# Kernel optimization log

Hardware: AMD Instinct MI355X
Metric: run time of the kernel (lower is better)

Reference implementation:

```python
import jax, jax.numpy as jnp
import numpy as np

N_NODES = 100000
N_EDGES = 1600000
N_FEAT = 128
N_HID = 128
N_CLASS = 10
N_GRAPHS = 512
BN_EPS = 1e-5


def setup_inputs() -> dict:
    key = jax.random.key(0)
    ks = jax.random.split(key, 12)
    x = jax.random.normal(ks[0], (N_NODES, N_FEAT), dtype=jnp.float32)
    edge_index = jax.random.randint(ks[1], (2, N_EDGES), 0, N_NODES, dtype=jnp.int32)
    batch = jnp.sort(jax.random.randint(ks[2], (N_NODES,), 0, N_GRAPHS, dtype=jnp.int32))
    s1 = 1.0 / np.sqrt(N_FEAT)
    s2 = 1.0 / np.sqrt(N_HID)
    W1 = jax.random.uniform(ks[3], (N_FEAT, N_HID), jnp.float32, -s1, s1)
    b1 = jax.random.uniform(ks[4], (N_HID,), jnp.float32, -s1, s1)
    gamma = jnp.ones((N_HID,), jnp.float32)
    beta = jnp.zeros((N_HID,), jnp.float32)
    W2 = jax.random.uniform(ks[5], (N_HID, N_HID), jnp.float32, -s2, s2)
    b2 = jax.random.uniform(ks[6], (N_HID,), jnp.float32, -s2, s2)
    clsW = jax.random.uniform(ks[7], (N_HID, N_CLASS), jnp.float32, -s2, s2)
    clsb = jax.random.uniform(ks[8], (N_CLASS,), jnp.float32, -s2, s2)
    return {"x": x, "edge_index": edge_index, "batch": batch,
            "W1": W1, "b1": b1, "gamma": gamma, "beta": beta,
            "W2": W2, "b2": b2, "clsW": clsW, "clsb": clsb}


def _gcn_norm(edge_index, n_nodes):
    # add self-loops, compute symmetric normalization D^-1/2 A_hat D^-1/2
    loops = jnp.arange(n_nodes, dtype=edge_index.dtype)
    src = jnp.concatenate([edge_index[0], loops])
    dst = jnp.concatenate([edge_index[1], loops])
    deg = jax.ops.segment_sum(jnp.ones_like(dst, dtype=jnp.float32), dst,
                              num_segments=n_nodes)
    dinv = jnp.where(deg > 0, jax.lax.rsqrt(deg), 0.0)
    norm = dinv[src] * dinv[dst]  # [E + N]
    return src, dst, norm


def _gcn_conv(h, src, dst, norm, W, b, n_nodes):
    h = h @ W                                   # [N, nhid] dense GEMM
    msg = h[src] * norm[:, None]                # gather + scale  [E+N, nhid]
    out = jax.ops.segment_sum(msg, dst, num_segments=n_nodes)  # scatter-add
    return out + b


def reference(x, edge_index, batch, W1, b1, gamma, beta, W2, b2, clsW, clsb):
    n_nodes = x.shape[0]
    src, dst, norm = _gcn_norm(edge_index, n_nodes)
    # layer 1: GCNConv -> BatchNorm(eval, running stats 0/1) -> ReLU -> Dropout(eval=id)
    h = _gcn_conv(x, src, dst, norm, W1, b1, n_nodes)
    h = h * (gamma / jnp.sqrt(1.0 + BN_EPS)) + beta
    h = jax.nn.relu(h)
    # layer 2: GCNConv (output layer, no bn/act)
    h = _gcn_conv(h, src, dst, norm, W2, b2, n_nodes)
    # global mean pool over batch index
    sums = jax.ops.segment_sum(h, batch, num_segments=N_GRAPHS)          # [G, nhid]
    cnts = jax.ops.segment_sum(jnp.ones((n_nodes,), h.dtype), batch,
                               num_segments=N_GRAPHS)
    g = sums / jnp.maximum(cnts, 1.0)[:, None]
    out = jax.nn.log_softmax(g @ clsW + clsb, axis=1)                    # [G, nclass]
    return out, g
```

## Files before the change

kernel.cpp:

```cpp
#include <hip/hip_runtime.h>
#include <hip/hip_bf16.h>

#define N_NODES 100000
#define N_EDGES 1600000
#define N_FEAT 128
#define N_HID 128
#define N_CLASS 10
#define N_GRAPHS 512
#define BN_RSQRT 0.9999950000374997f

#define NRANGE 12500
#define NSUB 512
#define SCAP 640
#define HGROUP 32
#define BPB (NSUB / HGROUP)

#define XT_STRIDE 136
#define YW_STRIDE 36
#define FG_LDS 78848

typedef _Float16 half_t;
typedef __attribute__((ext_vector_type(2))) _Float16 half2v;
typedef __attribute__((ext_vector_type(4))) _Float16 half4v;
typedef __attribute__((ext_vector_type(8))) _Float16 half8v;
typedef __attribute__((ext_vector_type(4))) float floatx4;
typedef __attribute__((ext_vector_type(2))) float floatx2;

__global__ __launch_bounds__(256) void bucket_fused(
    const int* __restrict__ src, const int* __restrict__ dst,
    int* __restrict__ cnt, unsigned long long* __restrict__ bucketed,
    const float* __restrict__ W1, half_t* __restrict__ Wt1,
    const float* __restrict__ W2, half_t* __restrict__ Wt2,
    const int* __restrict__ batch, int* __restrict__ boffs,
    int* __restrict__ sentinel,
    int chunkE, int E, int nnodes)
{
    __shared__ int wcnt[4][8];
    __shared__ int wbase[4][8];
    int blk = blockIdx.x;
    if (blk >= NSUB) {
        int k = blk - NSUB;
        if (k == 0) {
            if (threadIdx.x < 32) sentinel[threadIdx.x] = 0;
        } else if (k <= 128) {
            int i = (k - 1) * 256 + threadIdx.x;
            const float* W = (i < 16384) ? W1 : W2;
            half_t* Wt = (i < 16384) ? Wt1 : Wt2;
            int j = i & 16383;
            int c = j >> 7, kk = j & 127;
            Wt[(size_t)c * 128 + kk] = (half_t)W[(size_t)kk * 128 + c];
        } else {
            int i = (k - 129) * 256 + threadIdx.x;
            if (i < nnodes) {
                int b = batch[i];
                int prev = (i == 0) ? -1 : batch[i - 1];
                for (int g = prev + 1; g <= b; ++g) boffs[g] = i;
                if (i == nnodes - 1)
                    for (int g = b + 1; g <= N_GRAPHS; ++g) boffs[g] = nnodes;
            }
        }
        return;
    }
    int b = blk;
    int wave = threadIdx.x >> 6;
    int lane = threadIdx.x & 63;
    int e0 = b * chunkE;
    int e1 = e0 + chunkE < E ? e0 + chunkE : E;
    int iters = (chunkE + 255) / 256;

    int mycnt = 0;
    for (int it = 0; it < iters; ++it) {
        int e = e0 + it * 256 + threadIdx.x;
        bool valid = e < e1;
        int d = valid ? dst[e] : 0;
        int rr = (d * 8) / N_NODES;
#pragma unroll
        for (int r = 0; r < 8; ++r) {
            unsigned long long m = __ballot(valid && rr == r);
            if (lane == r) mycnt += __popcll(m);
        }
    }
    if (lane < 8) wcnt[wave][lane] = mycnt;
    __syncthreads();
    if (threadIdx.x < 8) {
        int r = threadIdx.x;
        int s = 0;
#pragma unroll
        for (int w = 0; w < 4; ++w) { wbase[w][r] = s; s += wcnt[w][r]; }
        cnt[r * NSUB + b] = s;
    }
    __syncthreads();

    int myoff = (lane < 8) ? wbase[wave][lane] : 0;
    for (int it = 0; it < iters; ++it) {
        int e = e0 + it * 256 + threadIdx.x;
        bool valid = e < e1;
        int s = valid ? src[e] : 0;
        int d = valid ? dst[e] : 0;
        int rr = (d * 8) / N_NODES;
        unsigned long long pk = ((unsigned long long)(unsigned)d << 32) | (unsigned)s;
#pragma unroll
        for (int r = 0; r < 8; ++r) {
            unsigned long long m = __ballot(valid && rr == r);
            int base_r = __shfl(myoff, r);
            if (valid && rr == r) {
                int pos = base_r + __popcll(m & ((1ull << lane) - 1));
                if (pos < SCAP)
                    bucketed[(size_t)(r * NSUB + b) * SCAP + pos] = pk;
            }
            if (lane == r) myoff += __popcll(m);
        }
    }
}

__global__ __launch_bounds__(256) void hist2(
    const unsigned long long* __restrict__ bucketed, const int* __restrict__ cnt,
    int* __restrict__ partial)
{
    __shared__ int h[NRANGE];
    int r = blockIdx.x & 7, g = blockIdx.x >> 3;
    for (int i = threadIdx.x; i < NRANGE; i += 256) h[i] = 0;
    __syncthreads();
    int rbase = r * NRANGE;
    for (int j = 0; j < BPB; ++j) {
        int b = g * BPB + j;
        int n = cnt[r * NSUB + b];
        if (n > SCAP) n = SCAP;
        const unsigned long long* seg = bucketed + (size_t)(r * NSUB + b) * SCAP;
        for (int i = threadIdx.x; i < n; i += 256)
            atomicAdd(&h[(int)(seg[i] >> 32) - rbase], 1);
    }
    __syncthreads();
    int* slice = partial + (size_t)(r * HGROUP + g) * NRANGE;
    for (int i = threadIdx.x; i < NRANGE; i += 256) slice[i] = h[i];
}

__global__ void deg_reduce(const int* __restrict__ partial, int* __restrict__ deg,
                           float* __restrict__ dinv, int* __restrict__ bsums, int n) {
    __shared__ int sm[256];
    int t = threadIdx.x;
    int i = blockIdx.x * 256 + t;
    int s = 0;
    if (i < n) {
        int rr = i / NRANGE;
        int dl = i - rr * NRANGE;
        const int* p = partial + (size_t)rr * HGROUP * NRANGE + dl;
#pragma unroll 8
        for (int g = 0; g < HGROUP; ++g) s += p[(size_t)g * NRANGE];
        deg[i] = s;
        dinv[i] = rsqrtf((float)s + 1.0f);
    }
    sm[t] = s;
    __syncthreads();
    for (int off = 128; off > 0; off >>= 1) {
        if (t < off) sm[t] += sm[t + off];
        __syncthreads();
    }
    if (t == 0) bsums[blockIdx.x] = sm[0];
}

__global__ void scan_small(int* __restrict__ bsums, int nb) {
    __shared__ int buf[1024];
    int t = threadIdx.x;
    int v = (t < nb) ? bsums[t] : 0;
    buf[t] = v;
    __syncthreads();
    for (int off = 1; off < 1024; off <<= 1) {
        int x = (t >= off) ? buf[t - off] : 0;
        __syncthreads();
        buf[t] += x;
        __syncthreads();
    }
    if (t < nb) bsums[t] = buf[t] - v;
}

__global__ __launch_bounds__(256) void scan_chunkoff(
    const int* __restrict__ in, const int* __restrict__ bsums,
    int* __restrict__ rowptr, int* __restrict__ partial, int n, int total)
{
    __shared__ int s[256];
    int t = threadIdx.x;
    int i = blockIdx.x * 256 + t;
    int v = (i < n) ? in[i] : 0;
    s[t] = v;
    __syncthreads();
    for (int off = 1; off < 256; off <<= 1) {
        int x = (t >= off) ? s[t - off] : 0;
        __syncthreads();
        s[t] += x;
        __syncthreads();
    }
    if (i == 0) rowptr[n] = total;
    if (i < n) {
        int excl = bsums[blockIdx.x] + s[t] - v;
        rowptr[i] = excl;
        int rr = i / NRANGE;
        int dl = i - rr * NRANGE;
        int* p = partial + (size_t)rr * HGROUP * NRANGE + dl;
        int vals[32];
#pragma unroll
        for (int g = 0; g < 32; ++g) vals[g] = p[(size_t)g * NRANGE];
        int running = excl;
#pragma unroll
        for (int g = 0; g < 32; ++g) {
            int tmp = vals[g];
            p[(size_t)g * NRANGE] = running;
            running += tmp;
        }
    }
}

__global__ __launch_bounds__(256, 2) void fill2_gemm1p(
    const unsigned long long* __restrict__ bucketed, const int* __restrict__ cnt,
    const int* __restrict__ partial, int* __restrict__ col,
    const float* __restrict__ X, const half_t* __restrict__ Wt,
    const float* __restrict__ dinv, unsigned char* __restrict__ Y8,
    int nrows, int ntiles)
{
    __shared__ __align__(16) unsigned char smem[FG_LDS];
    int tid = threadIdx.x;
    if (blockIdx.x < 256) {
        int* off = (int*)smem;
        int r = blockIdx.x & 7, g = blockIdx.x >> 3;
        const int* slice = partial + (size_t)(r * HGROUP + g) * NRANGE;
        for (int i = tid; i < NRANGE; i += 256) off[i] = slice[i];
        __syncthreads();
        int rbase = r * NRANGE;
        for (int j = 0; j < BPB; ++j) {
            int b = g * BPB + j;
            int n = cnt[r * NSUB + b];
            if (n > SCAP) n = SCAP;
            const unsigned long long* seg = bucketed + (size_t)(r * NSUB + b) * SCAP;
            for (int i = tid; i < n; i += 256) {
                unsigned long long pk = seg[i];
                int pos = atomicAdd(&off[(int)(pk >> 32) - rbase], 1);
                col[pos] = (int)((unsigned)(pk & 0xffffffffu) << 7);
            }
        }
        return;
    }
    half_t* wlds = (half_t*)smem;
    half_t* xb0  = (half_t*)(smem + 34816);
    half_t* xb1  = (half_t*)(smem + 52224);
    int* yw_all  = (int*)(smem + 69632);
    {
        const half8v* wg = (const half8v*)Wt;
        half8v w[8];
#pragma unroll
        for (int j = 0; j < 8; ++j) w[j] = wg[j * 256 + tid];
#pragma unroll
        for (int j = 0; j < 8; ++j) {
            int idx = j * 256 + tid;
            *(half8v*)(wlds + (idx >> 4) * XT_STRIDE + ((idx & 15) << 3)) = w[j];
        }
    }
    int wave = tid >> 6;
    int lane = tid & 63;
    int n16  = lane & 15;
    int quad = lane >> 4;
    int* yw = yw_all + wave * (16 * YW_STRIDE);
    int stride = gridDim.x - 256;

    int t = blockIdx.x - 256;
    if (t >= ntiles) return;
    half_t* xbc = xb0;
    half_t* xbn = xb1;
    {
        const float4* xg = (const float4*)(X + (size_t)t * 64 * 128);
        int idxmax = (nrows - t * 64) * 32;
#pragma unroll
        for (int j = 0; j < 8; ++j) {
            int idx = j * 256 + tid;
            if (idx < idxmax) {
                float4 f = xg[idx];
                half4v h = {(half_t)f.x, (half_t)f.y, (half_t)f.z, (half_t)f.w};
                *(half4v*)(xbc + (idx >> 5) * XT_STRIDE + ((idx & 31) << 2)) = h;
            }
        }
    }
    __syncthreads();
    for (;;) {
        int tn = t + stride;
        bool pf = tn < ntiles;
        float4 f[8];
        if (pf) {
            const float4* xg = (const float4*)(X + (size_t)tn * 64 * 128);
            int idxmax = (nrows - tn * 64) * 32;
#pragma unroll
            for (int j = 0; j < 8; ++j) {
                int idx = j * 256 + tid;
                f[j] = (idx < idxmax) ? xg[idx] : float4{0.f, 0.f, 0.f, 0.f};
            }
        }
        int r0 = t * 64 + wave * 16;
        bool active = r0 < nrows;
        int packedv[8];
        if (active) {
            const half_t* xr = xbc + (wave * 16 + n16) * XT_STRIDE;
            half8v a0 = *(const half8v*)(xr + 0 * 32 + quad * 8);
            half8v a1 = *(const half8v*)(xr + 1 * 32 + quad * 8);
            half8v a2 = *(const half8v*)(xr + 2 * 32 + quad * 8);
            half8v a3 = *(const half8v*)(xr + 3 * 32 + quad * 8);
            float dr = dinv[r0 + n16];
#pragma unroll
            for (int c = 0; c < 8; ++c) {
                const half_t* wl = wlds + (c * 16 + n16) * XT_STRIDE;
                floatx4 acc = {0.f, 0.f, 0.f, 0.f};
                acc = __builtin_amdgcn_mfma_f32_16x16x32_f16(*(const half8v*)(wl + 0 * 32 + quad * 8), a0, acc, 0, 0, 0);
                acc = __builtin_amdgcn_mfma_f32_16x16x32_f16(*(const half8v*)(wl + 1 * 32 + quad * 8), a1, acc, 0, 0, 0);
                acc = __builtin_amdgcn_mfma_f32_16x16x32_f16(*(const half8v*)(wl + 2 * 32 + quad * 8), a2, acc, 0, 0, 0);
                acc = __builtin_amdgcn_mfma_f32_16x16x32_f16(*(const half8v*)(wl + 3 * 32 + quad * 8), a3, acc, 0, 0, 0);
                int packed = __builtin_amdgcn_cvt_pk_fp8_f32(acc[0] * dr, acc[1] * dr, 0, false);
                packed = __builtin_amdgcn_cvt_pk_fp8_f32(acc[2] * dr, acc[3] * dr, packed, true);
                packedv[c] = packed;
            }
#pragma unroll
            for (int c = 0; c < 8; ++c)
                yw[n16 * YW_STRIDE + c * 4 + quad] = packedv[c];
#pragma unroll
            for (int u = 0; u < 2; ++u) {
                int4 v = *(const int4*)(yw + (u * 8 + (lane >> 3)) * YW_STRIDE + (lane & 7) * 4);
                *(int4*)(Y8 + (size_t)r0 * 128 + u * 1024 + lane * 16) = v;
            }
        }
        __syncthreads();
        if (!pf) break;
        {
            int idxmax = (nrows - tn * 64) * 32;
#pragma unroll
            for (int j = 0; j < 8; ++j) {
                int idx = j * 256 + tid;
                if (idx < idxmax) {
                    half4v h = {(half_t)f[j].x, (half_t)f[j].y, (half_t)f[j].z, (half_t)f[j].w};
                    *(half4v*)(xbn + (idx >> 5) * XT_STRIDE + ((idx & 31) << 2)) = h;
                }
            }
        }
        __syncthreads();
        half_t* tmp = xbc; xbc = xbn; xbn = tmp;
        t = tn;
    }
}

__global__ __launch_bounds__(256, 2) void gemm2_mfma(
    const half_t* __restrict__ X, const half_t* __restrict__ Wt,
    const float* __restrict__ dinv, unsigned char* __restrict__ Y8,
    int nrows, int ntiles)
{
    __shared__ __align__(16) half_t wlds[128 * XT_STRIDE];
    __shared__ __align__(16) half_t xb[2][64 * XT_STRIDE];
    __shared__ __align__(16) int yw_all[4 * 16 * YW_STRIDE];
    int tid = threadIdx.x;
    {
        const half8v* wg = (const half8v*)Wt;
        half8v w[8];
#pragma unroll
        for (int j = 0; j < 8; ++j) w[j] = wg[j * 256 + tid];
#pragma unroll
        for (int j = 0; j < 8; ++j) {
            int idx = j * 256 + tid;
            *(half8v*)(wlds + (idx >> 4) * XT_STRIDE + ((idx & 15) << 3)) = w[j];
        }
    }
    int wave = tid >> 6;
    int lane = tid & 63;
    int n16  = lane & 15;
    int quad = lane >> 4;
    int* yw = yw_all + wave * (16 * YW_STRIDE);

    int t = blockIdx.x;
    if (t >= ntiles) return;
    int cur = 0;
    {
        const half8v* xg = (const half8v*)(X + (size_t)t * 64 * 128);
        int idxmax = (nrows - t * 64) * 16;
#pragma unroll
        for (int j = 0; j < 4; ++j) {
            int idx = j * 256 + tid;
            if (idx < idxmax)
                *(half8v*)(xb[0] + (idx >> 4) * XT_STRIDE + ((idx & 15) << 3)) = xg[idx];
        }
    }
    __syncthreads();
    for (;;) {
        int tn = t + gridDim.x;
        bool pf = tn < ntiles;
        half8v v[4];
        if (pf) {
            const half8v* xg = (const half8v*)(X + (size_t)tn * 64 * 128);
            int idxmax = (nrows - tn * 64) * 16;
#pragma unroll
            for (int j = 0; j < 4; ++j) {
                int idx = j * 256 + tid;
                if (idx < idxmax) v[j] = xg[idx];
            }
        }
        int r0 = t * 64 + wave * 16;
        bool active = r0 < nrows;
        int packedv[8];
        if (active) {
            const half_t* xr = xb[cur] + (wave * 16 + n16) * XT_STRIDE;
            half8v a0 = *(const half8v*)(xr + 0 * 32 + quad * 8);
            half8v a1 = *(const half8v*)(xr + 1 * 32 + quad * 8);
            half8v a2 = *(const half8v*)(xr + 2 * 32 + quad * 8);
            half8v a3 = *(const half8v*)(xr + 3 * 32 + quad * 8);
            float dr = dinv[r0 + n16];
#pragma unroll
            for (int c = 0; c < 8; ++c) {
                const half_t* wl = wlds + (c * 16 + n16) * XT_STRIDE;
                floatx4 acc = {0.f, 0.f, 0.f, 0.f};
                acc = __builtin_amdgcn_mfma_f32_16x16x32_f16(*(const half8v*)(wl + 0 * 32 + quad * 8), a0, acc, 0, 0, 0);
                acc = __builtin_amdgcn_mfma_f32_16x16x32_f16(*(const half8v*)(wl + 1 * 32 + quad * 8), a1, acc, 0, 0, 0);
                acc = __builtin_amdgcn_mfma_f32_16x16x32_f16(*(const half8v*)(wl + 2 * 32 + quad * 8), a2, acc, 0, 0, 0);
                acc = __builtin_amdgcn_mfma_f32_16x16x32_f16(*(const half8v*)(wl + 3 * 32 + quad * 8), a3, acc, 0, 0, 0);
                int packed = __builtin_amdgcn_cvt_pk_fp8_f32(acc[0] * dr, acc[1] * dr, 0, false);
                packed = __builtin_amdgcn_cvt_pk_fp8_f32(acc[2] * dr, acc[3] * dr, packed, true);
                packedv[c] = packed;
            }
#pragma unroll
            for (int c = 0; c < 8; ++c)
                yw[n16 * YW_STRIDE + c * 4 + quad] = packedv[c];
#pragma unroll
            for (int u = 0; u < 2; ++u) {
                int4 o = *(const int4*)(yw + (u * 8 + (lane >> 3)) * YW_STRIDE + (lane & 7) * 4);
                *(int4*)(Y8 + (size_t)r0 * 128 + u * 1024 + lane * 16) = o;
            }
        }
        __syncthreads();
        if (!pf) break;
        {
            int idxmax = (nrows - tn * 64) * 16;
#pragma unroll
            for (int j = 0; j < 4; ++j) {
                int idx = j * 256 + tid;
                if (idx < idxmax)
                    *(half8v*)(xb[cur ^ 1] + (idx >> 4) * XT_STRIDE + ((idx & 15) << 3)) = v[j];
            }
        }
        __syncthreads();
        cur ^= 1;
        t = tn;
    }
}

__global__ __launch_bounds__(256, 4) void agg_fp8(
    const unsigned char* __restrict__ hs, half_t* __restrict__ out,
    const int* __restrict__ col, const int* __restrict__ rowptr,
    const float* __restrict__ bias,
    const float* __restrict__ gamma, const float* __restrict__ beta,
    int nnodes, int do_bn_relu)
{
    int wave = threadIdx.x >> 6;
    int lane = threadIdx.x & 63;
    int q = lane >> 4;
    int l16 = lane & 15;
    int nb4 = (blockIdx.x * 4 + wave) * 4;
    int i = nb4 + q;
    bool valid = i < nnodes;
    unsigned iq = valid ? (unsigned)i : (unsigned)nnodes;
    unsigned f8 = (unsigned)l16 << 3;
    unsigned ZOFF = (unsigned)nnodes << 7;

    int e0 = valid ? rowptr[i] : 0;
    int e1 = valid ? rowptr[i + 1] : 0;
    int deg = e1 - e0;
    int m = deg;
    m = max(m, __shfl_xor(m, 16));
    m = max(m, __shfl_xor(m, 32));
    int nchunk = (m + 15) >> 4;

    unsigned long long us = *(const unsigned long long*)(hs + ((iq << 7) | f8));

    floatx2 a0 = {0.f, 0.f}, a1 = {0.f, 0.f}, a2 = {0.f, 0.f}, a3 = {0.f, 0.f};
    for (int t = 0; t < nchunk; ++t) {
        int idx = e0 + t * 16 + l16;
        unsigned cv = (idx < e1) ? (unsigned)col[idx] : ZOFF;
#pragma unroll
        for (int half = 0; half < 2; ++half) {
            const int kk = half * 8;
            unsigned long long v0, v1, v2, v3, v4, v5, v6, v7;
#define AGG_ADDR(K)                                                            \
            ({ unsigned sA = (unsigned)__builtin_amdgcn_readlane((int)cv, kk + K);      \
               unsigned sB = (unsigned)__builtin_amdgcn_readlane((int)cv, kk + K + 16); \
               unsigned sC = (unsigned)__builtin_amdgcn_readlane((int)cv, kk + K + 32); \
               unsigned sD = (unsigned)__builtin_amdgcn_readlane((int)cv, kk + K + 48); \
               unsigned rAB = (q & 1) ? sB : sA;                               \
               unsigned rCD = (q & 1) ? sD : sC;                               \
               unsigned rr = (q & 2) ? rCD : rAB;                              \
               *(const unsigned long long*)(hs + (rr | f8)); })
            v0 = AGG_ADDR(0);
            v1 = AGG_ADDR(1);
            v2 = AGG_ADDR(2);
            v3 = AGG_ADDR(3);
            v4 = AGG_ADDR(4);
            v5 = AGG_ADDR(5);
            v6 = AGG_ADDR(6);
            v7 = AGG_ADDR(7);
#undef AGG_ADDR
#define AGG_ACC(V)                                                             \
            { unsigned lo = (unsigned)(V), hi = (unsigned)((V) >> 32);         \
              a0 += __builtin_amdgcn_cvt_pk_f32_fp8((int)lo, false);           \
              a1 += __builtin_amdgcn_cvt_pk_f32_fp8((int)lo, true);            \
              a2 += __builtin_amdgcn_cvt_pk_f32_fp8((int)hi, false);           \
              a3 += __builtin_amdgcn_cvt_pk_f32_fp8((int)hi, true); }
            AGG_ACC(v0) AGG_ACC(v1) AGG_ACC(v2) AGG_ACC(v3)
            AGG_ACC(v4) AGG_ACC(v5) AGG_ACC(v6) AGG_ACC(v7)
#undef AGG_ACC
        }
    }
    {
        unsigned lo = (unsigned)us, hi = (unsigned)(us >> 32);
        a0 += __builtin_amdgcn_cvt_pk_f32_fp8((int)lo, false);
        a1 += __builtin_amdgcn_cvt_pk_f32_fp8((int)lo, true);
        a2 += __builtin_amdgcn_cvt_pk_f32_fp8((int)hi, false);
        a3 += __builtin_amdgcn_cvt_pk_f32_fp8((int)hi, true);
    }

    if (!valid) return;
    float di = rsqrtf((float)deg + 1.0f);
    int fbase = l16 * 8;
    float4 bi0 = *(const float4*)(bias + fbase);
    float4 bi1 = *(const float4*)(bias + fbase + 4);
    float o0 = fmaf(di, a0.x, bi0.x);
    float o1 = fmaf(di, a0.y, bi0.y);
    float o2 = fmaf(di, a1.x, bi0.z);
    float o3 = fmaf(di, a1.y, bi0.w);
    float o4 = fmaf(di, a2.x, bi1.x);
    float o5 = fmaf(di, a2.y, bi1.y);
    float o6 = fmaf(di, a3.x, bi1.z);
    float o7 = fmaf(di, a3.y, bi1.w);
    if (do_bn_relu) {
        float4 ga0 = *(const float4*)(gamma + fbase);
        float4 ga1 = *(const float4*)(gamma + fbase + 4);
        float4 be0 = *(const float4*)(beta + fbase);
        float4 be1 = *(const float4*)(beta + fbase + 4);
        o0 = fmaf(o0, ga0.x * BN_RSQRT, be0.x);
        o1 = fmaf(o1, ga0.y * BN_RSQRT, be0.y);
        o2 = fmaf(o2, ga0.z * BN_RSQRT, be0.z);
        o3 = fmaf(o3, ga0.w * BN_RSQRT, be0.w);
        o4 = fmaf(o4, ga1.x * BN_RSQRT, be1.x);
        o5 = fmaf(o5, ga1.y * BN_RSQRT, be1.y);
        o6 = fmaf(o6, ga1.z * BN_RSQRT, be1.z);
        o7 = fmaf(o7, ga1.w * BN_RSQRT, be1.w);
        o0 = o0 > 0.f ? o0 : 0.f;
        o1 = o1 > 0.f ? o1 : 0.f;
        o2 = o2 > 0.f ? o2 : 0.f;
        o3 = o3 > 0.f ? o3 : 0.f;
        o4 = o4 > 0.f ? o4 : 0.f;
        o5 = o5 > 0.f ? o5 : 0.f;
        o6 = o6 > 0.f ? o6 : 0.f;
        o7 = o7 > 0.f ? o7 : 0.f;
    }
    half8v ov = {(half_t)o0, (half_t)o1, (half_t)o2, (half_t)o3,
                 (half_t)o4, (half_t)o5, (half_t)o6, (half_t)o7};
    *(half8v*)(out + (size_t)i * 128 + fbase) = ov;
}

__global__ __launch_bounds__(512) void pool_cls(
    const half_t* __restrict__ h, const int* __restrict__ boffs,
    const float* __restrict__ clsW, const float* __restrict__ clsb,
    float* __restrict__ gout, float* __restrict__ out)
{
    __shared__ float red[8][128];
    __shared__ float zbuf[16];
    int g = blockIdx.x;
    int w = threadIdx.x >> 6;
    int lane = threadIdx.x & 63;
    int n0 = boffs[g], n1 = boffs[g + 1];
    float ax = 0.f, ay = 0.f;
    for (int n = n0 + w; n < n1; n += 8) {
        half2v v = *(const half2v*)(h + (size_t)n * 128 + lane * 2);
        ax += (float)v.x;
        ay += (float)v.y;
    }
    red[w][lane * 2] = ax;
    red[w][lane * 2 + 1] = ay;
    __syncthreads();
    if (w == 0) {
        float sx = 0.f, sy = 0.f;
#pragma unroll
        for (int j = 0; j < 8; ++j) {
            sx += red[j][lane * 2];
            sy += red[j][lane * 2 + 1];
        }
        float cnt = (float)((n1 - n0) > 1 ? (n1 - n0) : 1);
        float g0 = sx / cnt, g1 = sy / cnt;
        gout[(size_t)g * 128 + lane * 2] = g0;
        gout[(size_t)g * 128 + lane * 2 + 1] = g1;
        red[0][lane * 2] = g0;
        red[0][lane * 2 + 1] = g1;
    }
    __syncthreads();
    if (threadIdx.x < N_CLASS) {
        int c = threadIdx.x;
        float z = clsb[c];
        for (int k = 0; k < N_HID; ++k)
            z = fmaf(red[0][k], clsW[k * N_CLASS + c], z);
        zbuf[c] = z;
    }
    __syncthreads();
    if (threadIdx.x == 0) {
        float m = zbuf[0];
#pragma unroll
        for (int c = 1; c < N_CLASS; ++c) m = fmaxf(m, zbuf[c]);
        float s = 0.f;
#pragma unroll
        for (int c = 0; c < N_CLASS; ++c) s += expf(zbuf[c] - m);
        float l = logf(s);
#pragma unroll
        for (int c = 0; c < N_CLASS; ++c)
            out[(size_t)g * N_CLASS + c] = zbuf[c] - m - l;
    }
}

extern "C" void kernel_launch(void* const* d_in, const int* in_sizes, int n_in,
                              void* d_out, int out_size, void* d_ws, size_t ws_size,
                              hipStream_t stream) {
    const float* x     = (const float*)d_in[0];
    const int*   ei    = (const int*)d_in[1];
    const int*   batch = (const int*)d_in[2];
    const float* W1    = (const float*)d_in[3];
    const float* b1    = (const float*)d_in[4];
    const float* gamma = (const float*)d_in[5];
    const float* beta  = (const float*)d_in[6];
    const float* W2    = (const float*)d_in[7];
    const float* b2    = (const float*)d_in[8];
    const float* clsW  = (const float*)d_in[9];
    const float* clsb  = (const float*)d_in[10];

    const int N = in_sizes[0] / N_FEAT;
    const int E = in_sizes[1] / 2;
    const int* src = ei;
    const int* dst = ei + E;

    unsigned char* BA8 = (unsigned char*)d_ws;
    half_t* BB = (half_t*)(BA8 + (size_t)(N + 1) * 128);
    half_t* Wt1 = BB + (size_t)N * 128;
    half_t* Wt2 = Wt1 + 16384;
    int*   col     = (int*)(Wt2 + 16384);
    int*   rowptr  = col + E;
    int*   deg     = rowptr + (N + 4);
    float* dinv    = (float*)(deg + N);
    int*   cnt     = (int*)(dinv + N);
    unsigned long long* bucketed =
        (unsigned long long*)(cnt + 8 * NSUB);
    int*   partial = (int*)(bucketed + (size_t)8 * NSUB * SCAP);
    int*   boffs   = partial + 8 * HGROUP * NRANGE;
    int*   bsums   = boffs + N_GRAPHS + 4;

    const int nb = (N + 255) / 256;
    const int chunkE = (E + NSUB - 1) / NSUB;
    const int ntiles = (N + 63) / 64;
    const int aggBlocks = (N + 15) / 16;

    bucket_fused<<<NSUB + 129 + nb, 256, 0, stream>>>(
        src, dst, cnt, bucketed, W1, Wt1, W2, Wt2, batch, boffs,
        (int*)(BA8 + (size_t)N * 128), chunkE, E, N);
    hist2<<<8 * HGROUP, 256, 0, stream>>>(bucketed, cnt, partial);
    deg_reduce<<<nb, 256, 0, stream>>>(partial, deg, dinv, bsums, N);
    scan_small<<<1, 1024, 0, stream>>>(bsums, nb);
    scan_chunkoff<<<nb, 256, 0, stream>>>(deg, bsums, rowptr, partial, N, E);
    fill2_gemm1p<<<256 + 512, 256, 0, stream>>>(
        bucketed, cnt, partial, col, x, Wt1, dinv, BA8, N, ntiles);
    agg_fp8<<<aggBlocks, 256, 0, stream>>>(BA8, BB, col, rowptr, b1, gamma, beta, N, 1);
    gemm2_mfma<<<512, 256, 0, stream>>>(BB, Wt2, dinv, BA8, N, ntiles);
    agg_fp8<<<aggBlocks, 256, 0, stream>>>(BA8, BB, col, rowptr, b2, gamma, beta, N, 0);

    float* out = (float*)d_out;
    float* gsec = out + (size_t)N_GRAPHS * N_CLASS;
    pool_cls<<<N_GRAPHS, 512, 0, stream>>>(BB, boffs, clsW, clsb, gsec, out);
}
```

Measured before the change: 281.0 us.

## Compute degrees with global atomics and overlap histogram pass with GEMM1

Degrees are now counted with global atomicAdd during bucketing, so dinv and rowptr can be computed before the per-subrange histogram. The histogram then runs in the same launch as the first GEMM, and the chunk offsets and CSR fill move to two new kernels after it. The aggregation kernel's four readlanes plus selects are replaced by a single __shfl. The cost is 1.6M contended global atomics, an extra memset and two extra launches, and the fill no longer overlaps with the GEMM.

```diff
diff --git a/kernel.cpp b/kernel.cpp
--- a/kernel.cpp
+++ b/kernel.cpp
@@ -29,6 +29,7 @@
 __global__ __launch_bounds__(256) void bucket_fused(
     const int* __restrict__ src, const int* __restrict__ dst,
     int* __restrict__ cnt, unsigned long long* __restrict__ bucketed,
+    int* __restrict__ deg,
     const float* __restrict__ W1, half_t* __restrict__ Wt1,
     const float* __restrict__ W2, half_t* __restrict__ Wt2,
     const int* __restrict__ batch, int* __restrict__ boffs,
@@ -73,6 +74,7 @@
         int e = e0 + it * 256 + threadIdx.x;
         bool valid = e < e1;
         int d = valid ? dst[e] : 0;
+        if (valid) atomicAdd(&deg[d], 1);
         int rr = (d * 8) / N_NODES;
 #pragma unroll
         for (int r = 0; r < 8; ++r) {
@@ -113,41 +115,16 @@
     }
 }
 
-__global__ __launch_bounds__(256) void hist2(
-    const unsigned long long* __restrict__ bucketed, const int* __restrict__ cnt,
-    int* __restrict__ partial)
-{
-    __shared__ int h[NRANGE];
-    int r = blockIdx.x & 7, g = blockIdx.x >> 3;
-    for (int i = threadIdx.x; i < NRANGE; i += 256) h[i] = 0;
-    __syncthreads();
-    int rbase = r * NRANGE;
-    for (int j = 0; j < BPB; ++j) {
-        int b = g * BPB + j;
-        int n = cnt[r * NSUB + b];
-        if (n > SCAP) n = SCAP;
-        const unsigned long long* seg = bucketed + (size_t)(r * NSUB + b) * SCAP;
-        for (int i = threadIdx.x; i < n; i += 256)
-            atomicAdd(&h[(int)(seg[i] >> 32) - rbase], 1);
-    }
-    __syncthreads();
-    int* slice = partial + (size_t)(r * HGROUP + g) * NRANGE;
-    for (int i = threadIdx.x; i < NRANGE; i += 256) slice[i] = h[i];
-}
-
-__global__ void deg_reduce(const int* __restrict__ partial, int* __restrict__ deg,
-                           float* __restrict__ dinv, int* __restrict__ bsums, int n) {
+__global__ __launch_bounds__(256) void dinv_bsums(
+    const int* __restrict__ deg, float* __restrict__ dinv,
+    int* __restrict__ bsums, int n)
+{
     __shared__ int sm[256];
     int t = threadIdx.x;
     int i = blockIdx.x * 256 + t;
     int s = 0;
     if (i < n) {
-        int rr = i / NRANGE;
-        int dl = i - rr * NRANGE;
-        const int* p = partial + (size_t)rr * HGROUP * NRANGE + dl;
-#pragma unroll 8
-        for (int g = 0; g < HGROUP; ++g) s += p[(size_t)g * NRANGE];
-        deg[i] = s;
+        s = deg[i];
         dinv[i] = rsqrtf((float)s + 1.0f);
     }
     sm[t] = s;
@@ -174,9 +151,9 @@
     if (t < nb) bsums[t] = buf[t] - v;
 }
 
-__global__ __launch_bounds__(256) void scan_chunkoff(
+__global__ __launch_bounds__(256) void scan_final_rowptr(
     const int* __restrict__ in, const int* __restrict__ bsums,
-    int* __restrict__ rowptr, int* __restrict__ partial, int n, int total)
+    int* __restrict__ rowptr, int n, int total)
 {
     __shared__ int s[256];
     int t = threadIdx.x;
@@ -191,28 +168,12 @@
         __syncthreads();
     }
     if (i == 0) rowptr[n] = total;
-    if (i < n) {
-        int excl = bsums[blockIdx.x] + s[t] - v;
-        rowptr[i] = excl;
-        int rr = i / NRANGE;
-        int dl = i - rr * NRANGE;
-        int* p = partial + (size_t)rr * HGROUP * NRANGE + dl;
-        int vals[32];
-#pragma unroll
-        for (int g = 0; g < 32; ++g) vals[g] = p[(size_t)g * NRANGE];
-        int running = excl;
-#pragma unroll
-        for (int g = 0; g < 32; ++g) {
-            int tmp = vals[g];
-            p[(size_t)g * NRANGE] = running;
-            running += tmp;
-        }
-    }
-}
-
-__global__ __launch_bounds__(256, 2) void fill2_gemm1p(
+    if (i < n) rowptr[i] = bsums[blockIdx.x] + s[t] - v;
+}
+
+__global__ __launch_bounds__(256, 2) void hist2_gemm1p(
     const unsigned long long* __restrict__ bucketed, const int* __restrict__ cnt,
-    const int* __restrict__ partial, int* __restrict__ col,
+    int* __restrict__ partial,
     const float* __restrict__ X, const half_t* __restrict__ Wt,
     const float* __restrict__ dinv, unsigned char* __restrict__ Y8,
     int nrows, int ntiles)
@@ -220,10 +181,9 @@
     __shared__ __align__(16) unsigned char smem[FG_LDS];
     int tid = threadIdx.x;
     if (blockIdx.x < 256) {
-        int* off = (int*)smem;
+        int* h = (int*)smem;
         int r = blockIdx.x & 7, g = blockIdx.x >> 3;
-        const int* slice = partial + (size_t)(r * HGROUP + g) * NRANGE;
-        for (int i = tid; i < NRANGE; i += 256) off[i] = slice[i];
+        for (int i = tid; i < NRANGE; i += 256) h[i] = 0;
         __syncthreads();
         int rbase = r * NRANGE;
         for (int j = 0; j < BPB; ++j) {
@@ -231,12 +191,12 @@
             int n = cnt[r * NSUB + b];
             if (n > SCAP) n = SCAP;
             const unsigned long long* seg = bucketed + (size_t)(r * NSUB + b) * SCAP;
-            for (int i = tid; i < n; i += 256) {
-                unsigned long long pk = seg[i];
-                int pos = atomicAdd(&off[(int)(pk >> 32) - rbase], 1);
-                col[pos] = (int)((unsigned)(pk & 0xffffffffu) << 7);
-            }
-        }
+            for (int i = tid; i < n; i += 256)
+                atomicAdd(&h[(int)(seg[i] >> 32) - rbase], 1);
+        }
+        __syncthreads();
+        int* slice = partial + (size_t)(r * HGROUP + g) * NRANGE;
+        for (int i = tid; i < NRANGE; i += 256) slice[i] = h[i];
         return;
     }
     half_t* wlds = (half_t*)smem;
@@ -342,6 +302,49 @@
     }
 }
 
+__global__ __launch_bounds__(256) void chunkoff2(
+    const int* __restrict__ rowptr, int* __restrict__ partial, int n)
+{
+    int i = blockIdx.x * 256 + threadIdx.x;
+    if (i >= n) return;
+    int rr = i / NRANGE;
+    int dl = i - rr * NRANGE;
+    int* p = partial + (size_t)rr * HGROUP * NRANGE + dl;
+    int vals[32];
+#pragma unroll
+    for (int g = 0; g < 32; ++g) vals[g] = p[(size_t)g * NRANGE];
+    int running = rowptr[i];
+#pragma unroll
+    for (int g = 0; g < 32; ++g) {
+        int tmp = vals[g];
+        p[(size_t)g * NRANGE] = running;
+        running += tmp;
+    }
+}
+
+__global__ __launch_bounds__(256) void fill2(
+    const unsigned long long* __restrict__ bucketed, const int* __restrict__ cnt,
+    const int* __restrict__ partial, int* __restrict__ col)
+{
+    __shared__ int off[NRANGE];
+    int r = blockIdx.x & 7, g = blockIdx.x >> 3;
+    const int* slice = partial + (size_t)(r * HGROUP + g) * NRANGE;
+    for (int i = threadIdx.x; i < NRANGE; i += 256) off[i] = slice[i];
+    __syncthreads();
+    int rbase = r * NRANGE;
+    for (int j = 0; j < BPB; ++j) {
+        int b = g * BPB + j;
+        int n = cnt[r * NSUB + b];
+        if (n > SCAP) n = SCAP;
+        const unsigned long long* seg = bucketed + (size_t)(r * NSUB + b) * SCAP;
+        for (int i = threadIdx.x; i < n; i += 256) {
+            unsigned long long pk = seg[i];
+            int pos = atomicAdd(&off[(int)(pk >> 32) - rbase], 1);
+            col[pos] = (int)((unsigned)(pk & 0xffffffffu) << 7);
+        }
+    }
+}
+
 __global__ __launch_bounds__(256, 2) void gemm2_mfma(
     const half_t* __restrict__ X, const half_t* __restrict__ Wt,
     const float* __restrict__ dinv, unsigned char* __restrict__ Y8,
@@ -453,6 +456,7 @@
     int wave = threadIdx.x >> 6;
     int lane = threadIdx.x & 63;
     int q = lane >> 4;
+    int q16 = lane & 48;
     int l16 = lane & 15;
     int nb4 = (blockIdx.x * 4 + wave) * 4;
     int i = nb4 + q;
@@ -480,13 +484,7 @@
             const int kk = half * 8;
             unsigned long long v0, v1, v2, v3, v4, v5, v6, v7;
 #define AGG_ADDR(K)                                                            \
-            ({ unsigned sA = (unsigned)__builtin_amdgcn_readlane((int)cv, kk + K);      \
-               unsigned sB = (unsigned)__builtin_amdgcn_readlane((int)cv, kk + K + 16); \
-               unsigned sC = (unsigned)__builtin_amdgcn_readlane((int)cv, kk + K + 32); \
-               unsigned sD = (unsigned)__builtin_amdgcn_readlane((int)cv, kk + K + 48); \
-               unsigned rAB = (q & 1) ? sB : sA;                               \
-               unsigned rCD = (q & 1) ? sD : sC;                               \
-               unsigned rr = (q & 2) ? rCD : rAB;                              \
+            ({ unsigned rr = (unsigned)__shfl((int)cv, kk + K + q16);          \
                *(const unsigned long long*)(hs + (rr | f8)); })
             v0 = AGG_ADDR(0);
             v1 = AGG_ADDR(1);
@@ -653,15 +651,18 @@
     const int ntiles = (N + 63) / 64;
     const int aggBlocks = (N + 15) / 16;
 
+    hipMemsetAsync(deg, 0, (size_t)N * sizeof(int), stream);
+
     bucket_fused<<<NSUB + 129 + nb, 256, 0, stream>>>(
-        src, dst, cnt, bucketed, W1, Wt1, W2, Wt2, batch, boffs,
+        src, dst, cnt, bucketed, deg, W1, Wt1, W2, Wt2, batch, boffs,
         (int*)(BA8 + (size_t)N * 128), chunkE, E, N);
-    hist2<<<8 * HGROUP, 256, 0, stream>>>(bucketed, cnt, partial);
-    deg_reduce<<<nb, 256, 0, stream>>>(partial, deg, dinv, bsums, N);
+    dinv_bsums<<<nb, 256, 0, stream>>>(deg, dinv, bsums, N);
     scan_small<<<1, 1024, 0, stream>>>(bsums, nb);
-    scan_chunkoff<<<nb, 256, 0, stream>>>(deg, bsums, rowptr, partial, N, E);
-    fill2_gemm1p<<<256 + 512, 256, 0, stream>>>(
-        bucketed, cnt, partial, col, x, Wt1, dinv, BA8, N, ntiles);
+    scan_final_rowptr<<<nb, 256, 0, stream>>>(deg, bsums, rowptr, N, E);
+    hist2_gemm1p<<<256 + 512, 256, 0, stream>>>(
+        bucketed, cnt, partial, x, Wt1, dinv, BA8, N, ntiles);
+    chunkoff2<<<nb, 256, 0, stream>>>(rowptr, partial, N);
+    fill2<<<256, 256, 0, stream>>>(bucketed, cnt, partial, col);
     agg_fp8<<<aggBlocks, 256, 0, stream>>>(BA8, BB, col, rowptr, b1, gamma, beta, N, 1);
     gemm2_mfma<<<512, 256, 0, stream>>>(BB, Wt2, dinv, BA8, N, ntiles);
     agg_fp8<<<aggBlocks, 256, 0, stream>>>(BA8, BB, col, rowptr, b2, gamma, beta, N, 0);
```

Measured after the change: 342.3 us. 1.22x slower.
